# Kernel tuning notes

Hardware: AMD Instinct MI355X
Metric: run time of the kernel (lower is better)

Reference implementation:

```python
import jax, jax.numpy as jnp
import numpy as np

B, T_DEC, U, T_K, D, V = 32, 64, 32, 64, 512, 50257


def setup_inputs() -> dict:
    key = jax.random.key(0)
    ks = jax.random.split(key, 24)
    s = 0.02  # weight init scale
    inp = {
        "target_features": jax.random.normal(ks[0], (B, T_DEC, D), jnp.float32),
        "target_mask": jnp.ones((B, T_DEC), jnp.float32),
        "encode_features": jax.random.normal(ks[1], (B, U, D), jnp.float32),
        "utterance_mask": jnp.ones((B, U), jnp.float32),
        "token_features": jax.random.normal(ks[2], (U, B, T_K, D), jnp.float32),
        "token_mask": jnp.ones((U, B, T_K), jnp.float32),
        "coverage": jnp.zeros((B, U), jnp.float32),
        "token_coverage": jnp.zeros((U, B, T_K), jnp.float32),
        # utterance_attention params
        "ua_Wp": jax.random.normal(ks[3], (D, D), jnp.float32) * s,
        "ua_bp": jnp.zeros((D,), jnp.float32),
        "ua_v": jax.random.normal(ks[4], (D,), jnp.float32) * s,
        "ua_wc": jax.random.normal(ks[5], (D,), jnp.float32) * s,  # W_c: Linear(1,D) weight, squeezed
        # token_attention params
        "ta_Wp": jax.random.normal(ks[6], (D, D), jnp.float32) * s,
        "ta_bp": jnp.zeros((D,), jnp.float32),
        "ta_v": jax.random.normal(ks[7], (D,), jnp.float32) * s,
        "ta_wc": jax.random.normal(ks[8], (D,), jnp.float32) * s,
        # pointer-gen + output projections
        "pgen_W": jax.random.normal(ks[9], (1, 2 * D), jnp.float32) * s,
        "pgen_b": jnp.zeros((1,), jnp.float32),
        "out1_W": jax.random.normal(ks[10], (D, 2 * D), jnp.float32) * s,
        "out1_b": jnp.zeros((D,), jnp.float32),
        "out2_W": jax.random.normal(ks[11], (V, D), jnp.float32) * s,
        "out2_b": jnp.zeros((V,), jnp.float32),
        # LayerNorm params
        "ln_g": jnp.ones((D,), jnp.float32),
        "ln_b": jnp.zeros((D,), jnp.float32),
    }
    return inp


def _local_attn(t, enc, mask, cov, Wp, bp, v, wc):
    # t: [..., D] decoder state, enc: [..., T, D], mask/cov: [..., T]
    dec = t @ Wp.T + bp                                   # [..., D]
    att = enc + dec[..., None, :] + cov[..., None] * wc   # additive + coverage feature
    scores = jnp.einsum('...td,d->...t', jnp.tanh(att), v)
    attn_ = jax.nn.softmax(scores, axis=-1) * mask
    nf = attn_.sum(-1, keepdims=True)
    attn = attn_ / jnp.where(nf == 0, 1.0, nf)
    out = jnp.einsum('...t,...td->...d', attn, enc)       # context vector
    return out, attn, cov + attn


def reference(target_features, target_mask, encode_features, utterance_mask,
              token_features, token_mask, coverage, token_coverage,
              ua_Wp, ua_bp, ua_v, ua_wc, ta_Wp, ta_bp, ta_v, ta_wc,
              pgen_W, pgen_b, out1_W, out1_b, out2_W, out2_b, ln_g, ln_b):
    # layers == [] so the transformer-layer loop is a no-op; then LayerNorm.
    mu = target_features.mean(-1, keepdims=True)
    var = ((target_features - mu) ** 2).mean(-1, keepdims=True)
    normed = (target_features - mu) * jax.lax.rsqrt(var + 1e-5) * ln_g + ln_b
    local_dec = normed[:, -1, :]                           # [B, D]

    # utterance-level attention
    u_out, u_attn, u_cov = _local_attn(local_dec, encode_features, utterance_mask,
                                       coverage, ua_Wp, ua_bp, ua_v, ua_wc)

    # per-utterance token attention, batched over U (replaces Python for-loop)
    tok = jax.vmap(lambda e, m, c: _local_attn(local_dec, e, m, c, ta_Wp, ta_bp, ta_v, ta_wc))
    utters_out, utters_attn, next_tok_cov = tok(token_features, token_mask, token_coverage)
    # utters_out: [U, B, D], utters_attn/next_tok_cov: [U, B, T_K]

    p_gen = jax.nn.sigmoid(jnp.concatenate([u_out, local_dec], axis=1) @ pgen_W.T + pgen_b)

    # topk(k=1) == argmax (first max on ties, matching torch.topk)
    utter_index = jnp.argmax(u_attn, axis=1)               # [B]
    idx = jnp.arange(u_attn.shape[0])
    target_attn_dist = utters_attn[utter_index, idx, :]    # [B, T_K]
    target_out = utters_out[utter_index, idx, :]           # [B, D]

    h = jnp.concatenate([target_out, local_dec], axis=1) @ out1_W.T + out1_b
    logits = h @ out2_W.T + out2_b
    vocab_dist = jax.nn.softmax(logits, axis=1)
    return vocab_dist, target_attn_dist, p_gen, u_cov, next_tok_cov, utter_index
```

## Files before the change

### kernel.cpp

```cpp
#include <hip/hip_runtime.h>
#include <math.h>

#define BB 32
#define TDEC 64
#define UU 32
#define TK 64
#define DD 512
#define VV 50257
#define NT5 3142
#define K5_GRID 1024

#define WS_LDEC   0
#define WS_DEC_U  16384
#define WS_DEC_T  32768
#define WS_UATTN  49152
#define WS_UIDX   50176
#define WS_TSC    50208
#define WS_TATTN  115744
#define WS_TOUT   181280
#define WS_H      197664
#define WS_PSUM   214048
#define WS_SUMS   246816

#define OUT_VOCAB 0
#define OUT_TAD   1608224
#define OUT_PGEN  1610272
#define OUT_UCOV  1610304
#define OUT_NTC   1611328
#define OUT_UIDX  1676864

__device__ __forceinline__ float wave_sum(float v) {
    #pragma unroll
    for (int off = 32; off > 0; off >>= 1) v += __shfl_xor(v, off, 64);
    return v;
}
__device__ __forceinline__ float wave_max(float v) {
    #pragma unroll
    for (int off = 32; off > 0; off >>= 1) v = fmaxf(v, __shfl_xor(v, off, 64));
    return v;
}
__device__ __forceinline__ float fast_tanh(float x) {
    float e2 = __expf(2.0f * x);
    return 1.0f - 2.0f * __builtin_amdgcn_rcpf(e2 + 1.0f);
}

__global__ __launch_bounds__(256) void k1_ln_proj(
    const float* __restrict__ tf, const float* __restrict__ ln_g, const float* __restrict__ ln_b,
    const float* __restrict__ ua_Wp, const float* __restrict__ ua_bp,
    const float* __restrict__ ta_Wp, const float* __restrict__ ta_bp,
    float* __restrict__ ws)
{
    int b = blockIdx.x >> 3, slice = blockIdx.x & 7;
    int tid = threadIdx.x, wid = tid >> 6, lane = tid & 63;
    __shared__ __align__(16) float ldec[DD];
    __shared__ float red[4];
    const float* x = tf + ((size_t)b * TDEC + (TDEC - 1)) * DD;
    float x0 = x[tid], x1 = x[tid + 256];

    float s = wave_sum(x0 + x1);
    if (lane == 0) red[wid] = s;
    __syncthreads();
    float mean = (red[0] + red[1] + red[2] + red[3]) * (1.0f / DD);
    __syncthreads();
    float d0 = x0 - mean, d1 = x1 - mean;
    s = wave_sum(d0 * d0 + d1 * d1);
    if (lane == 0) red[wid] = s;
    __syncthreads();
    float var = (red[0] + red[1] + red[2] + red[3]) * (1.0f / DD);
    float inv = rsqrtf(var + 1e-5f);
    float n0 = d0 * inv * ln_g[tid] + ln_b[tid];
    float n1 = d1 * inv * ln_g[tid + 256] + ln_b[tid + 256];
    ldec[tid] = n0; ldec[tid + 256] = n1;
    if (slice == 0) {
        ws[WS_LDEC + b * DD + tid] = n0;
        ws[WS_LDEC + b * DD + tid + 256] = n1;
    }
    __syncthreads();

    int r = slice * 128 + (tid >> 1);
    int m = r >> 9, rr = r & 511;
    int kh = tid & 1;
    const float* Wp = m ? ta_Wp : ua_Wp;
    const float* bp = m ? ta_bp : ua_bp;
    const float4* wr = (const float4*)(Wp + (size_t)rr * DD + kh * 256);
    const float4* hl = (const float4*)ldec + kh * 64;
    float acc = 0.f;
    #pragma unroll 8
    for (int i = 0; i < 64; i++) {
        float4 w = wr[i]; float4 h = hl[i];
        acc += w.x * h.x + w.y * h.y + w.z * h.z + w.w * h.w;
    }
    float tot = acc + __shfl_xor(acc, 1, 64);
    if (kh == 0) {
        float* dst = ws + (m ? WS_DEC_T : WS_DEC_U) + b * DD + rr;
        *dst = tot + bp[rr];
    }
}

__global__ __launch_bounds__(256) void k2_uattn(
    const float* __restrict__ enc, const float* __restrict__ umask,
    const float* __restrict__ cov, const float* __restrict__ ua_v,
    const float* __restrict__ ua_wc, const float* __restrict__ pgen_W,
    const float* __restrict__ pgen_b,
    float* __restrict__ ws, float* __restrict__ out)
{
    int b = blockIdx.x, tid = threadIdx.x, wid = tid >> 6, lane = tid & 63;
    __shared__ __align__(16) float decu[DD], wcl[DD], vvl[DD], ldec[DD], uo[DD];
    __shared__ float sc[UU], attn[UU], red[4];
    decu[tid] = ws[WS_DEC_U + b * DD + tid]; decu[tid + 256] = ws[WS_DEC_U + b * DD + tid + 256];
    wcl[tid] = ua_wc[tid]; wcl[tid + 256] = ua_wc[tid + 256];
    vvl[tid] = ua_v[tid];  vvl[tid + 256] = ua_v[tid + 256];
    ldec[tid] = ws[WS_LDEC + b * DD + tid]; ldec[tid + 256] = ws[WS_LDEC + b * DD + tid + 256];
    __syncthreads();

    for (int u = wid; u < UU; u += 4) {
        float cb = cov[b * UU + u];
        const float* e = enc + ((size_t)b * UU + u) * DD;
        float p = 0.f;
        #pragma unroll
        for (int i = 0; i < DD / 64; i++) {
            int d = lane + i * 64;
            p += fast_tanh(e[d] + decu[d] + cb * wcl[d]) * vvl[d];
        }
        p = wave_sum(p);
        if (lane == 0) sc[u] = p;
    }
    __syncthreads();

    if (tid < 64) {
        float s = (tid < UU) ? sc[tid] : -INFINITY;
        float m = wave_max(s);
        float e = (tid < UU) ? __expf(s - m) : 0.f;
        float sum = wave_sum(e);
        float a_ = (e / sum) * ((tid < UU) ? umask[b * UU + tid] : 0.f);
        float nf = wave_sum(a_);
        float a = a_ / (nf == 0.f ? 1.f : nf);
        float av = (tid < UU) ? a : -INFINITY;
        float am = wave_max(av);
        unsigned long long ball = __ballot(av == am);
        int idx = __ffsll(ball) - 1;
        if (tid < UU) {
            attn[tid] = a;
            ws[WS_UATTN + b * UU + tid] = a;
            out[OUT_UCOV + b * UU + tid] = cov[b * UU + tid] + a;
        }
        if (tid == 0) {
            ((int*)ws)[WS_UIDX + b] = idx;
            out[OUT_UIDX + b] = (float)idx;
        }
    }
    __syncthreads();

    for (int d = tid; d < DD; d += 256) {
        float s = 0.f;
        #pragma unroll
        for (int u = 0; u < UU; u++) s += attn[u] * enc[((size_t)b * UU + u) * DD + d];
        uo[d] = s;
    }
    __syncthreads();

    float pp = uo[tid] * pgen_W[tid] + uo[tid + 256] * pgen_W[tid + 256]
             + ldec[tid] * pgen_W[DD + tid] + ldec[tid + 256] * pgen_W[DD + tid + 256];
    pp = wave_sum(pp);
    if (lane == 0) red[wid] = pp;
    __syncthreads();
    if (tid == 0) {
        float t = red[0] + red[1] + red[2] + red[3] + pgen_b[0];
        out[OUT_PGEN + b] = 1.f / (1.f + __expf(-t));
    }
}

__global__ __launch_bounds__(256, 4) void k3a_tscore(
    const float* __restrict__ tok, const float* __restrict__ tcov,
    const float* __restrict__ ta_v, const float* __restrict__ ta_wc,
    float* __restrict__ ws)
{
    int blk = blockIdx.x;
    int u = blk >> 6, r = blk & 63, b = r >> 1, hf = r & 1;
    int tid = threadIdx.x, wid = tid >> 6, lane = tid & 63;

    const float4* dec4 = (const float4*)(ws + WS_DEC_T + b * DD);
    const float4* wc4  = (const float4*)ta_wc;
    const float4* vv4  = (const float4*)ta_v;
    float4 dc0 = dec4[lane], dc1 = dec4[lane + 64];
    float4 wc0 = wc4[lane],  wc1 = wc4[lane + 64];
    float4 vv0 = vv4[lane],  vv1 = vv4[lane + 64];

    const float* base = tok + ((size_t)(u * BB + b)) * TK * DD;
    const float* tcb  = tcov + (size_t)(u * BB + b) * TK;
    int t0 = hf * 32 + wid * 8;

    float4 x[8][2];
    float tc[8];
    #pragma unroll
    for (int j = 0; j < 8; j++) {
        const float4* row = (const float4*)(base + (size_t)(t0 + j) * DD);
        x[j][0] = row[lane];
        x[j][1] = row[lane + 64];
        tc[j] = tcb[t0 + j];
    }
    #pragma unroll
    for (int j = 0; j < 8; j++) {
        float p = 0.f;
        float4 a = x[j][0], c = x[j][1];
        float t_ = tc[j];
        p += fast_tanh(a.x + dc0.x + t_ * wc0.x) * vv0.x;
        p += fast_tanh(a.y + dc0.y + t_ * wc0.y) * vv0.y;
        p += fast_tanh(a.z + dc0.z + t_ * wc0.z) * vv0.z;
        p += fast_tanh(a.w + dc0.w + t_ * wc0.w) * vv0.w;
        p += fast_tanh(c.x + dc1.x + t_ * wc1.x) * vv1.x;
        p += fast_tanh(c.y + dc1.y + t_ * wc1.y) * vv1.y;
        p += fast_tanh(c.z + dc1.z + t_ * wc1.z) * vv1.z;
        p += fast_tanh(c.w + dc1.w + t_ * wc1.w) * vv1.w;
        p = wave_sum(p);
        if (lane == 0) ws[WS_TSC + (size_t)(u * BB + b) * TK + t0 + j] = p;
    }
}

__global__ __launch_bounds__(256) void k3b_tsoftmax(
    const float* __restrict__ tmask, const float* __restrict__ tcov,
    float* __restrict__ ws, float* __restrict__ out)
{
    int tid = threadIdx.x, wid = tid >> 6, lane = tid & 63;
    int g = blockIdx.x * 4 + wid;
    float s = ws[WS_TSC + (size_t)g * TK + lane];
    float m = wave_max(s);
    float e = __expf(s - m);
    float sum = wave_sum(e);
    float a_ = (e / sum) * tmask[(size_t)g * TK + lane];
    float nf = wave_sum(a_);
    float a = a_ / (nf == 0.f ? 1.f : nf);
    ws[WS_TATTN + (size_t)g * TK + lane] = a;
    out[OUT_NTC + (size_t)g * TK + lane] = tcov[(size_t)g * TK + lane] + a;
}

__global__ __launch_bounds__(256) void k4a_gather(
    const float* __restrict__ tok, float* __restrict__ ws, float* __restrict__ out)
{
    int b = blockIdx.x, tid = threadIdx.x;
    __shared__ float at[TK];
    int u = ((const int*)ws)[WS_UIDX + b];
    if (tid < TK) {
        float a = ws[WS_TATTN + (size_t)(u * BB + b) * TK + tid];
        at[tid] = a;
        out[OUT_TAD + b * TK + tid] = a;
    }
    __syncthreads();
    const float* base = tok + ((size_t)(u * BB + b)) * TK * DD;
    float a0 = 0.f, a1 = 0.f;
    #pragma unroll 8
    for (int t = 0; t < TK; t++) {
        float a = at[t];
        a0 += a * base[(size_t)t * DD + tid];
        a1 += a * base[(size_t)t * DD + tid + 256];
    }
    ws[WS_TOUT + b * DD + tid] = a0;
    ws[WS_TOUT + b * DD + tid + 256] = a1;
}

__global__ __launch_bounds__(256) void k4b_h(
    const float* __restrict__ out1_W, const float* __restrict__ out1_b,
    float* __restrict__ ws)
{
    int slice = blockIdx.x >> 5, b = blockIdx.x & 31;
    int tid = threadIdx.x;
    __shared__ __align__(16) float hcat[2 * DD];
    hcat[tid]       = ws[WS_TOUT + b * DD + tid];
    hcat[tid + 256] = ws[WS_TOUT + b * DD + tid + 256];
    hcat[tid + 512] = ws[WS_LDEC + b * DD + tid];
    hcat[tid + 768] = ws[WS_LDEC + b * DD + tid + 256];
    __syncthreads();

    int row = slice * 128 + (tid >> 1);
    int kh = tid & 1;
    const float4* wr = (const float4*)(out1_W + (size_t)row * (2 * DD) + kh * 512);
    const float4* hl = (const float4*)hcat + kh * 128;
    float acc = 0.f;
    #pragma unroll 8
    for (int i = 0; i < 128; i++) {
        float4 w = wr[i]; float4 h = hl[i];
        acc += w.x * h.x + w.y * h.y + w.z * h.z + w.w * h.w;
    }
    float tot = acc + __shfl_xor(acc, 1, 64);
    if (kh == 0) ws[WS_H + b * DD + row] = tot + out1_b[row];
}

__global__ __launch_bounds__(512, 4) void k5_gemv(
    const float* __restrict__ W2, const float* __restrict__ b2,
    float* __restrict__ ws, float* __restrict__ out)
{
    int tid = threadIdx.x;
    int b = tid & 31, kc = tid >> 5;
    __shared__ float red[16 * 16 * 33];
    float4 hr[8];
    {
        const float4* hp = (const float4*)(ws + WS_H + b * DD + kc * 32);
        #pragma unroll
        for (int i = 0; i < 8; i++) hr[i] = hp[i];
    }
    int jj = tid & 15, bb = tid >> 4;
    float es = 0.f;

    for (int tile = blockIdx.x; tile < NT5; tile += K5_GRID) {
        int v0 = tile * 16;
        float acc[16];
        #pragma unroll
        for (int j = 0; j < 16; j++) acc[j] = 0.f;
        #pragma unroll 2
        for (int j = 0; j < 16; j++) {
            int v = v0 + j;
            if (v < VV) {
                const float4* wr = (const float4*)(W2 + (size_t)v * DD + kc * 32);
                float a = 0.f;
                #pragma unroll
                for (int i = 0; i < 8; i++) {
                    float4 w = wr[i];
                    a += w.x * hr[i].x + w.y * hr[i].y + w.z * hr[i].z + w.w * hr[i].w;
                }
                acc[j] = a;
            }
        }
        #pragma unroll
        for (int j = 0; j < 16; j++) red[(kc * 16 + j) * 33 + b] = acc[j];
        __syncthreads();
        {
            int v = v0 + jj;
            if (v < VV) {
                float s = 0.f;
                #pragma unroll
                for (int k = 0; k < 16; k++) s += red[(k * 16 + jj) * 33 + bb];
                float e = __expf(s + b2[v]);
                out[(size_t)bb * VV + v] = e;
                es += e;
            }
        }
        __syncthreads();
    }
    #pragma unroll
    for (int off = 1; off < 16; off <<= 1) es += __shfl_xor(es, off, 64);
    if (jj == 0) ws[WS_PSUM + blockIdx.x * 32 + bb] = es;
}

__global__ __launch_bounds__(256) void k_sum(float* __restrict__ ws)
{
    int tid = threadIdx.x;
    int b = tid & 31, c = tid >> 5;
    __shared__ float red8[8][32];
    float p = 0.f;
    for (int g = c * 128; g < (c + 1) * 128; g++) p += ws[WS_PSUM + g * 32 + b];
    red8[c][b] = p;
    __syncthreads();
    if (tid < 32) {
        float s = 0.f;
        #pragma unroll
        for (int c2 = 0; c2 < 8; c2++) s += red8[c2][tid];
        ws[WS_SUMS + tid] = 1.0f / s;
    }
}

__global__ __launch_bounds__(256) void k_scale(const float* __restrict__ ws, float* __restrict__ out)
{
    int b = blockIdx.y;
    int v = blockIdx.x * 256 + threadIdx.x;
    if (v < VV) out[(size_t)b * VV + v] *= ws[WS_SUMS + b];
}

extern "C" void kernel_launch(void* const* d_in, const int* in_sizes, int n_in,
                              void* d_out, int out_size, void* d_ws, size_t ws_size,
                              hipStream_t stream) {
    const float* tf      = (const float*)d_in[0];
    const float* enc     = (const float*)d_in[2];
    const float* umask   = (const float*)d_in[3];
    const float* tok     = (const float*)d_in[4];
    const float* tmask   = (const float*)d_in[5];
    const float* cov     = (const float*)d_in[6];
    const float* tcov    = (const float*)d_in[7];
    const float* ua_Wp   = (const float*)d_in[8];
    const float* ua_bp   = (const float*)d_in[9];
    const float* ua_v    = (const float*)d_in[10];
    const float* ua_wc   = (const float*)d_in[11];
    const float* ta_Wp   = (const float*)d_in[12];
    const float* ta_bp   = (const float*)d_in[13];
    const float* ta_v    = (const float*)d_in[14];
    const float* ta_wc   = (const float*)d_in[15];
    const float* pgen_W  = (const float*)d_in[16];
    const float* pgen_b  = (const float*)d_in[17];
    const float* out1_W  = (const float*)d_in[18];
    const float* out1_b  = (const float*)d_in[19];
    const float* out2_W  = (const float*)d_in[20];
    const float* out2_b  = (const float*)d_in[21];
    const float* ln_g    = (const float*)d_in[22];
    const float* ln_b    = (const float*)d_in[23];

    float* ws  = (float*)d_ws;
    float* out = (float*)d_out;

    k1_ln_proj<<<dim3(256), dim3(256), 0, stream>>>(tf, ln_g, ln_b, ua_Wp, ua_bp, ta_Wp, ta_bp, ws);
    k2_uattn<<<dim3(BB), dim3(256), 0, stream>>>(enc, umask, cov, ua_v, ua_wc, pgen_W, pgen_b, ws, out);
    k3a_tscore<<<dim3(2048), dim3(256), 0, stream>>>(tok, tcov, ta_v, ta_wc, ws);
    k3b_tsoftmax<<<dim3(256), dim3(256), 0, stream>>>(tmask, tcov, ws, out);
    k4a_gather<<<dim3(BB), dim3(256), 0, stream>>>(tok, ws, out);
    k4b_h<<<dim3(128), dim3(256), 0, stream>>>(out1_W, out1_b, ws);
    k5_gemv<<<dim3(K5_GRID), dim3(512), 0, stream>>>(out2_W, out2_b, ws, out);
    k_sum<<<dim3(1), dim3(256), 0, stream>>>(ws);
    k_scale<<<dim3(197, 32), dim3(256), 0, stream>>>(ws, out);
}
```

Measured before the change: 475.4 us.

## Restructure vocab GEMV, fuse token score+softmax, vectorize attention kernels

Several changes land together. The vocab projection kernel now gives each thread one vocab row, keeps a transposed h (512x32) in LDS and accumulates all 32 batch outputs in registers, so W2 is read once with no cross-thread LDS reduction per tile. Token scoring and token softmax are fused into one kernel per (u,b), which removes the score round-trip through workspace and one launch. The utterance-attention and gather kernels switch to float4 loads with split-K partial sums. The GEMV runs only 393 blocks of 128 threads with 64KB LDS and 32 accumulators per thread, so occupancy is low, and each thread reads its own 2KB row, so loads across a wave are strided and poorly coalesced.

```diff
diff --git a/kernel.cpp b/kernel.cpp
--- a/kernel.cpp
+++ b/kernel.cpp
@@ -7,20 +7,20 @@
 #define TK 64
 #define DD 512
 #define VV 50257
-#define NT5 3142
-#define K5_GRID 1024
+#define K5_TPB 128
+#define K5_GRID 393
+#define NPSUM (K5_GRID * 2)
 
 #define WS_LDEC   0
 #define WS_DEC_U  16384
 #define WS_DEC_T  32768
 #define WS_UATTN  49152
 #define WS_UIDX   50176
-#define WS_TSC    50208
-#define WS_TATTN  115744
-#define WS_TOUT   181280
-#define WS_H      197664
-#define WS_PSUM   214048
-#define WS_SUMS   246816
+#define WS_TATTN  50208
+#define WS_TOUT   115744
+#define WS_H      132128
+#define WS_PSUM   148512
+#define WS_SUMS   173664
 
 #define OUT_VOCAB 0
 #define OUT_TAD   1608224
@@ -105,22 +105,30 @@
     float* __restrict__ ws, float* __restrict__ out)
 {
     int b = blockIdx.x, tid = threadIdx.x, wid = tid >> 6, lane = tid & 63;
-    __shared__ __align__(16) float decu[DD], wcl[DD], vvl[DD], ldec[DD], uo[DD];
+    __shared__ __align__(16) float4 decu4[128], wcl4[128], vvl4[128], ldec4[128];
+    __shared__ __align__(16) float4 part[2][128], uo4[128];
     __shared__ float sc[UU], attn[UU], red[4];
-    decu[tid] = ws[WS_DEC_U + b * DD + tid]; decu[tid + 256] = ws[WS_DEC_U + b * DD + tid + 256];
-    wcl[tid] = ua_wc[tid]; wcl[tid + 256] = ua_wc[tid + 256];
-    vvl[tid] = ua_v[tid];  vvl[tid + 256] = ua_v[tid + 256];
-    ldec[tid] = ws[WS_LDEC + b * DD + tid]; ldec[tid + 256] = ws[WS_LDEC + b * DD + tid + 256];
+
+    if (tid < 128) {
+        decu4[tid] = ((const float4*)(ws + WS_DEC_U + b * DD))[tid];
+        wcl4[tid]  = ((const float4*)ua_wc)[tid];
+        vvl4[tid]  = ((const float4*)ua_v)[tid];
+        ldec4[tid] = ((const float4*)(ws + WS_LDEC + b * DD))[tid];
+    }
     __syncthreads();
 
     for (int u = wid; u < UU; u += 4) {
         float cb = cov[b * UU + u];
-        const float* e = enc + ((size_t)b * UU + u) * DD;
+        const float4* e4 = (const float4*)(enc + ((size_t)b * UU + u) * DD);
         float p = 0.f;
         #pragma unroll
-        for (int i = 0; i < DD / 64; i++) {
-            int d = lane + i * 64;
-            p += fast_tanh(e[d] + decu[d] + cb * wcl[d]) * vvl[d];
+        for (int i = 0; i < 2; i++) {
+            int idx = lane + i * 64;
+            float4 x = e4[idx], dc = decu4[idx], wc = wcl4[idx], vv = vvl4[idx];
+            p += fast_tanh(x.x + dc.x + cb * wc.x) * vv.x;
+            p += fast_tanh(x.y + dc.y + cb * wc.y) * vv.y;
+            p += fast_tanh(x.z + dc.z + cb * wc.z) * vv.z;
+            p += fast_tanh(x.w + dc.w + cb * wc.w) * vv.w;
         }
         p = wave_sum(p);
         if (lane == 0) sc[u] = p;
@@ -151,16 +159,38 @@
     }
     __syncthreads();
 
-    for (int d = tid; d < DD; d += 256) {
-        float s = 0.f;
-        #pragma unroll
-        for (int u = 0; u < UU; u++) s += attn[u] * enc[((size_t)b * UU + u) * DD + d];
-        uo[d] = s;
-    }
-    __syncthreads();
-
-    float pp = uo[tid] * pgen_W[tid] + uo[tid + 256] * pgen_W[tid + 256]
-             + ldec[tid] * pgen_W[DD + tid] + ldec[tid + 256] * pgen_W[DD + tid + 256];
+    {
+        int cid = tid & 127, half = tid >> 7;
+        const float4* e4 = (const float4*)(enc + (size_t)b * UU * DD);
+        float4 s = {0.f, 0.f, 0.f, 0.f};
+        #pragma unroll
+        for (int uu = 0; uu < 16; uu++) {
+            int u = half * 16 + uu;
+            float a = attn[u];
+            float4 x = e4[(size_t)u * 128 + cid];
+            s.x += a * x.x; s.y += a * x.y; s.z += a * x.z; s.w += a * x.w;
+        }
+        part[half][cid] = s;
+    }
+    __syncthreads();
+    if (tid < 128) {
+        float4 p0 = part[0][tid], p1 = part[1][tid];
+        float4 r = {p0.x + p1.x, p0.y + p1.y, p0.z + p1.z, p0.w + p1.w};
+        uo4[tid] = r;
+    }
+    __syncthreads();
+
+    float pp;
+    if (tid < 128) {
+        float4 v = uo4[tid];
+        float4 pw = ((const float4*)pgen_W)[tid];
+        pp = v.x * pw.x + v.y * pw.y + v.z * pw.z + v.w * pw.w;
+    } else {
+        int t2 = tid - 128;
+        float4 v = ldec4[t2];
+        float4 pw = ((const float4*)pgen_W)[128 + t2];
+        pp = v.x * pw.x + v.y * pw.y + v.z * pw.z + v.w * pw.w;
+    }
     pp = wave_sum(pp);
     if (lane == 0) red[wid] = pp;
     __syncthreads();
@@ -170,14 +200,16 @@
     }
 }
 
-__global__ __launch_bounds__(256, 4) void k3a_tscore(
-    const float* __restrict__ tok, const float* __restrict__ tcov,
-    const float* __restrict__ ta_v, const float* __restrict__ ta_wc,
-    float* __restrict__ ws)
-{
-    int blk = blockIdx.x;
-    int u = blk >> 6, r = blk & 63, b = r >> 1, hf = r & 1;
+__global__ __launch_bounds__(256) void k3_fused(
+    const float* __restrict__ tok, const float* __restrict__ tmask,
+    const float* __restrict__ tcov, const float* __restrict__ ta_v,
+    const float* __restrict__ ta_wc,
+    float* __restrict__ ws, float* __restrict__ out)
+{
+    int g = blockIdx.x;
+    int b = g & 31;
     int tid = threadIdx.x, wid = tid >> 6, lane = tid & 63;
+    __shared__ float sc[TK];
 
     const float4* dec4 = (const float4*)(ws + WS_DEC_T + b * DD);
     const float4* wc4  = (const float4*)ta_wc;
@@ -186,52 +218,51 @@
     float4 wc0 = wc4[lane],  wc1 = wc4[lane + 64];
     float4 vv0 = vv4[lane],  vv1 = vv4[lane + 64];
 
-    const float* base = tok + ((size_t)(u * BB + b)) * TK * DD;
-    const float* tcb  = tcov + (size_t)(u * BB + b) * TK;
-    int t0 = hf * 32 + wid * 8;
-
-    float4 x[8][2];
-    float tc[8];
-    #pragma unroll
-    for (int j = 0; j < 8; j++) {
-        const float4* row = (const float4*)(base + (size_t)(t0 + j) * DD);
-        x[j][0] = row[lane];
-        x[j][1] = row[lane + 64];
-        tc[j] = tcb[t0 + j];
-    }
-    #pragma unroll
-    for (int j = 0; j < 8; j++) {
-        float p = 0.f;
-        float4 a = x[j][0], c = x[j][1];
-        float t_ = tc[j];
-        p += fast_tanh(a.x + dc0.x + t_ * wc0.x) * vv0.x;
-        p += fast_tanh(a.y + dc0.y + t_ * wc0.y) * vv0.y;
-        p += fast_tanh(a.z + dc0.z + t_ * wc0.z) * vv0.z;
-        p += fast_tanh(a.w + dc0.w + t_ * wc0.w) * vv0.w;
-        p += fast_tanh(c.x + dc1.x + t_ * wc1.x) * vv1.x;
-        p += fast_tanh(c.y + dc1.y + t_ * wc1.y) * vv1.y;
-        p += fast_tanh(c.z + dc1.z + t_ * wc1.z) * vv1.z;
-        p += fast_tanh(c.w + dc1.w + t_ * wc1.w) * vv1.w;
-        p = wave_sum(p);
-        if (lane == 0) ws[WS_TSC + (size_t)(u * BB + b) * TK + t0 + j] = p;
-    }
-}
-
-__global__ __launch_bounds__(256) void k3b_tsoftmax(
-    const float* __restrict__ tmask, const float* __restrict__ tcov,
-    float* __restrict__ ws, float* __restrict__ out)
-{
-    int tid = threadIdx.x, wid = tid >> 6, lane = tid & 63;
-    int g = blockIdx.x * 4 + wid;
-    float s = ws[WS_TSC + (size_t)g * TK + lane];
-    float m = wave_max(s);
-    float e = __expf(s - m);
-    float sum = wave_sum(e);
-    float a_ = (e / sum) * tmask[(size_t)g * TK + lane];
-    float nf = wave_sum(a_);
-    float a = a_ / (nf == 0.f ? 1.f : nf);
-    ws[WS_TATTN + (size_t)g * TK + lane] = a;
-    out[OUT_NTC + (size_t)g * TK + lane] = tcov[(size_t)g * TK + lane] + a;
+    const float* base = tok + (size_t)g * TK * DD;
+    const float* tcb  = tcov + (size_t)g * TK;
+
+    #pragma unroll
+    for (int grp = 0; grp < 4; grp++) {
+        int t0 = wid * 16 + grp * 4;
+        float4 x0[4], x1[4];
+        float tc[4];
+        #pragma unroll
+        for (int j = 0; j < 4; j++) {
+            const float4* row = (const float4*)(base + (size_t)(t0 + j) * DD);
+            x0[j] = row[lane];
+            x1[j] = row[lane + 64];
+            tc[j] = tcb[t0 + j];
+        }
+        #pragma unroll
+        for (int j = 0; j < 4; j++) {
+            float t_ = tc[j];
+            float4 a = x0[j], c = x1[j];
+            float p = 0.f;
+            p += fast_tanh(a.x + dc0.x + t_ * wc0.x) * vv0.x;
+            p += fast_tanh(a.y + dc0.y + t_ * wc0.y) * vv0.y;
+            p += fast_tanh(a.z + dc0.z + t_ * wc0.z) * vv0.z;
+            p += fast_tanh(a.w + dc0.w + t_ * wc0.w) * vv0.w;
+            p += fast_tanh(c.x + dc1.x + t_ * wc1.x) * vv1.x;
+            p += fast_tanh(c.y + dc1.y + t_ * wc1.y) * vv1.y;
+            p += fast_tanh(c.z + dc1.z + t_ * wc1.z) * vv1.z;
+            p += fast_tanh(c.w + dc1.w + t_ * wc1.w) * vv1.w;
+            p = wave_sum(p);
+            if (lane == 0) sc[t0 + j] = p;
+        }
+    }
+    __syncthreads();
+
+    if (tid < 64) {
+        float s = sc[tid];
+        float m = wave_max(s);
+        float e = __expf(s - m);
+        float sum = wave_sum(e);
+        float a_ = (e / sum) * tmask[(size_t)g * TK + tid];
+        float nf = wave_sum(a_);
+        float a = a_ / (nf == 0.f ? 1.f : nf);
+        ws[WS_TATTN + (size_t)g * TK + tid] = a;
+        out[OUT_NTC + (size_t)g * TK + tid] = tcb[tid] + a;
+    }
 }
 
 __global__ __launch_bounds__(256) void k4a_gather(
@@ -239,6 +270,7 @@
 {
     int b = blockIdx.x, tid = threadIdx.x;
     __shared__ float at[TK];
+    __shared__ __align__(16) float4 part[2][128];
     int u = ((const int*)ws)[WS_UIDX + b];
     if (tid < TK) {
         float a = ws[WS_TATTN + (size_t)(u * BB + b) * TK + tid];
@@ -246,16 +278,23 @@
         out[OUT_TAD + b * TK + tid] = a;
     }
     __syncthreads();
-    const float* base = tok + ((size_t)(u * BB + b)) * TK * DD;
-    float a0 = 0.f, a1 = 0.f;
+    const float4* base4 = (const float4*)(tok + ((size_t)(u * BB + b)) * TK * DD);
+    int cid = tid & 127, th = tid >> 7;
+    float4 s = {0.f, 0.f, 0.f, 0.f};
     #pragma unroll 8
-    for (int t = 0; t < TK; t++) {
+    for (int tt = 0; tt < 32; tt++) {
+        int t = th * 32 + tt;
         float a = at[t];
-        a0 += a * base[(size_t)t * DD + tid];
-        a1 += a * base[(size_t)t * DD + tid + 256];
-    }
-    ws[WS_TOUT + b * DD + tid] = a0;
-    ws[WS_TOUT + b * DD + tid + 256] = a1;
+        float4 x = base4[(size_t)t * 128 + cid];
+        s.x += a * x.x; s.y += a * x.y; s.z += a * x.z; s.w += a * x.w;
+    }
+    part[th][cid] = s;
+    __syncthreads();
+    if (tid < 128) {
+        float4 p0 = part[0][tid], p1 = part[1][tid];
+        float4 r = {p0.x + p1.x, p0.y + p1.y, p0.z + p1.z, p0.w + p1.w};
+        ((float4*)(ws + WS_TOUT + b * DD))[tid] = r;
+    }
 }
 
 __global__ __launch_bounds__(256) void k4b_h(
@@ -285,60 +324,70 @@
     if (kh == 0) ws[WS_H + b * DD + row] = tot + out1_b[row];
 }
 
-__global__ __launch_bounds__(512, 4) void k5_gemv(
+__global__ __launch_bounds__(128) void k5_gemv(
     const float* __restrict__ W2, const float* __restrict__ b2,
     float* __restrict__ ws, float* __restrict__ out)
 {
-    int tid = threadIdx.x;
-    int b = tid & 31, kc = tid >> 5;
-    __shared__ float red[16 * 16 * 33];
-    float4 hr[8];
+    __shared__ __align__(16) float hT[DD * 32];
+    int tid = threadIdx.x, wid = tid >> 6;
+
     {
-        const float4* hp = (const float4*)(ws + WS_H + b * DD + kc * 32);
-        #pragma unroll
-        for (int i = 0; i < 8; i++) hr[i] = hp[i];
-    }
-    int jj = tid & 15, bb = tid >> 4;
-    float es = 0.f;
-
-    for (int tile = blockIdx.x; tile < NT5; tile += K5_GRID) {
-        int v0 = tile * 16;
-        float acc[16];
-        #pragma unroll
-        for (int j = 0; j < 16; j++) acc[j] = 0.f;
-        #pragma unroll 2
-        for (int j = 0; j < 16; j++) {
-            int v = v0 + j;
-            if (v < VV) {
-                const float4* wr = (const float4*)(W2 + (size_t)v * DD + kc * 32);
-                float a = 0.f;
-                #pragma unroll
-                for (int i = 0; i < 8; i++) {
-                    float4 w = wr[i];
-                    a += w.x * hr[i].x + w.y * hr[i].y + w.z * hr[i].z + w.w * hr[i].w;
-                }
-                acc[j] = a;
+        int bb = tid >> 2;
+        int kq = (tid & 3) * 128;
+        const float4* hp = (const float4*)(ws + WS_H + bb * DD + kq);
+        #pragma unroll
+        for (int i = 0; i < 32; i++) {
+            float4 hv = hp[i];
+            int k = kq + i * 4;
+            hT[(k + 0) * 32 + bb] = hv.x;
+            hT[(k + 1) * 32 + bb] = hv.y;
+            hT[(k + 2) * 32 + bb] = hv.z;
+            hT[(k + 3) * 32 + bb] = hv.w;
+        }
+    }
+    __syncthreads();
+
+    int v = blockIdx.x * K5_TPB + tid;
+    bool valid = v < VV;
+    int vld = valid ? v : (VV - 1);
+    const float4* wrow = (const float4*)(W2 + (size_t)vld * DD);
+
+    float acc[32];
+    #pragma unroll
+    for (int i = 0; i < 32; i++) acc[i] = 0.f;
+
+    #pragma unroll 4
+    for (int kt = 0; kt < 128; kt++) {
+        float4 w = wrow[kt];
+        #pragma unroll
+        for (int kk = 0; kk < 4; kk++) {
+            float wk = (kk == 0) ? w.x : (kk == 1) ? w.y : (kk == 2) ? w.z : w.w;
+            const float4* hrow = (const float4*)&hT[(kt * 4 + kk) * 32];
+            #pragma unroll
+            for (int b0 = 0; b0 < 8; b0++) {
+                float4 hb = hrow[b0];
+                acc[b0 * 4 + 0] += wk * hb.x;
+                acc[b0 * 4 + 1] += wk * hb.y;
+                acc[b0 * 4 + 2] += wk * hb.z;
+                acc[b0 * 4 + 3] += wk * hb.w;
             }
         }
-        #pragma unroll
-        for (int j = 0; j < 16; j++) red[(kc * 16 + j) * 33 + b] = acc[j];
-        __syncthreads();
-        {
-            int v = v0 + jj;
-            if (v < VV) {
-                float s = 0.f;
-                #pragma unroll
-                for (int k = 0; k < 16; k++) s += red[(k * 16 + jj) * 33 + bb];
-                float e = __expf(s + b2[v]);
-                out[(size_t)bb * VV + v] = e;
-                es += e;
-            }
-        }
-        __syncthreads();
-    }
-    #pragma unroll
-    for (int off = 1; off < 16; off <<= 1) es += __shfl_xor(es, off, 64);
-    if (jj == 0) ws[WS_PSUM + blockIdx.x * 32 + bb] = es;
+    }
+
+    float bias = valid ? b2[v] : 0.f;
+    #pragma unroll
+    for (int b = 0; b < 32; b++) {
+        float e = valid ? __expf(acc[b] + bias) : 0.f;
+        acc[b] = e;
+        if (valid) out[(size_t)b * VV + v] = e;
+    }
+    #pragma unroll
+    for (int b = 0; b < 32; b++) acc[b] = wave_sum(acc[b]);
+    if ((tid & 63) == 0) {
+        float* ps = ws + WS_PSUM + ((size_t)blockIdx.x * 2 + wid) * 32;
+        #pragma unroll
+        for (int b = 0; b < 32; b++) ps[b] = acc[b];
+    }
 }
 
 __global__ __launch_bounds__(256) void k_sum(float* __restrict__ ws)
@@ -347,7 +396,9 @@
     int b = tid & 31, c = tid >> 5;
     __shared__ float red8[8][32];
     float p = 0.f;
-    for (int g = c * 128; g < (c + 1) * 128; g++) p += ws[WS_PSUM + g * 32 + b];
+    int g0 = c * 99, g1 = (c + 1) * 99;
+    if (g1 > NPSUM) g1 = NPSUM;
+    for (int g = g0; g < g1; g++) p += ws[WS_PSUM + g * 32 + b];
     red8[c][b] = p;
     __syncthreads();
     if (tid < 32) {
@@ -397,11 +448,10 @@
 
     k1_ln_proj<<<dim3(256), dim3(256), 0, stream>>>(tf, ln_g, ln_b, ua_Wp, ua_bp, ta_Wp, ta_bp, ws);
     k2_uattn<<<dim3(BB), dim3(256), 0, stream>>>(enc, umask, cov, ua_v, ua_wc, pgen_W, pgen_b, ws, out);
-    k3a_tscore<<<dim3(2048), dim3(256), 0, stream>>>(tok, tcov, ta_v, ta_wc, ws);
-    k3b_tsoftmax<<<dim3(256), dim3(256), 0, stream>>>(tmask, tcov, ws, out);
+    k3_fused<<<dim3(UU * BB), dim3(256), 0, stream>>>(tok, tmask, tcov, ta_v, ta_wc, ws, out);
     k4a_gather<<<dim3(BB), dim3(256), 0, stream>>>(tok, ws, out);
     k4b_h<<<dim3(128), dim3(256), 0, stream>>>(out1_W, out1_b, ws);
-    k5_gemv<<<dim3(K5_GRID), dim3(512), 0, stream>>>(out2_W, out2_b, ws, out);
+    k5_gemv<<<dim3(K5_GRID), dim3(K5_TPB), 0, stream>>>(out2_W, out2_b, ws, out);
     k_sum<<<dim3(1), dim3(256), 0, stream>>>(ws);
     k_scale<<<dim3(197, 32), dim3(256), 0, stream>>>(ws, out);
 }
```

After: 413.9 us. -12.9%, faster.
